# Kernel optimization log

Measured on AMD Instinct MI355X. Metric: run time of the kernel, lower is better.

Reference implementation:

```python
import jax, jax.numpy as jnp
import numpy as np

D_MODEL = 1024
NUM_HEADS = 16
HEAD_DIM = D_MODEL // NUM_HEADS
MAX_SEQ_LEN = 2048
THETA = 10000.0
B, T = 2, 2048


def precompute_cos_sin(head_dim, max_len, theta):
    freqs = 1.0 / theta ** (jnp.arange(0, head_dim, 2, dtype=jnp.float32) / head_dim)
    t = jnp.arange(max_len, dtype=jnp.float32)
    f = jnp.outer(t, freqs)  # [max_len, head_dim//2]
    return jnp.concatenate([jnp.cos(f), jnp.sin(f)], axis=-1)  # [max_len, head_dim]


def apply_rotary_emb(x, cos_sin):
    # x: [B, H, T, Hs]; cos_sin: [T, Hs]
    xr = x.reshape(*x.shape[:-1], -1, 2)
    x1, x2 = xr[..., 0], xr[..., 1]
    cos, sin = jnp.split(cos_sin, 2, axis=-1)  # each [T, Hs//2]
    out = jnp.stack([x1 * cos - x2 * sin, x1 * sin + x2 * cos], axis=-1)
    return out.reshape(x.shape).astype(x.dtype)


def setup_inputs() -> dict:
    key = jax.random.key(0)
    ks = jax.random.split(key, 5)
    scale = 1.0 / np.sqrt(D_MODEL)
    return {
        'x': jax.random.normal(ks[0], (B, T, D_MODEL), dtype=jnp.float32),
        'wq': jax.random.normal(ks[1], (D_MODEL, D_MODEL), dtype=jnp.float32) * scale,
        'wk': jax.random.normal(ks[2], (D_MODEL, D_MODEL), dtype=jnp.float32) * scale,
        'wv': jax.random.normal(ks[3], (D_MODEL, D_MODEL), dtype=jnp.float32) * scale,
        'wo': jax.random.normal(ks[4], (D_MODEL, D_MODEL), dtype=jnp.float32) * scale,
    }


def reference(x, wq, wk, wv, wo):
    seq_len = x.shape[1]
    # Linear: einsum('...i,oi->...o'), weight stored as [out, in]
    q = jnp.einsum('bti,oi->bto', x, wq)
    k = jnp.einsum('bti,oi->bto', x, wk)
    v = jnp.einsum('bti,oi->bto', x, wv)
    # split heads: B T (nH Hs) -> B nH T Hs
    def split_heads(t):
        return t.reshape(t.shape[0], t.shape[1], NUM_HEADS, HEAD_DIM).transpose(0, 2, 1, 3)
    xq, xk, xv = split_heads(q), split_heads(k), split_heads(v)
    cos_sin = precompute_cos_sin(HEAD_DIM, MAX_SEQ_LEN, THETA)[:seq_len]
    xq = apply_rotary_emb(xq, cos_sin)
    xk = apply_rotary_emb(xk, cos_sin)
    scores = jnp.einsum('bhqd,bhkd->bhqk', xq, xk) / jnp.sqrt(jnp.float32(HEAD_DIM))
    causal = jnp.tril(jnp.ones((seq_len, seq_len), dtype=bool))
    scores = jnp.where(causal[None, None], scores, -jnp.inf)
    attn = jax.nn.softmax(scores, axis=-1)
    xo = jnp.einsum('bhqk,bhkd->bhqd', attn, xv)
    xo = xo.transpose(0, 2, 1, 3).reshape(x.shape[0], seq_len, D_MODEL)
    return jnp.einsum('bti,oi->bto', xo, wo)
```

## Files before the change

### kernel.cpp

```cpp
#include <hip/hip_runtime.h>
#include <hip/hip_bf16.h>

typedef __hip_bfloat16 bf16;
using s8v = __attribute__((ext_vector_type(8))) short;
using s4v = __attribute__((ext_vector_type(4))) short;
using f4v = __attribute__((ext_vector_type(4))) float;

#define D_MODEL 1024
#define NHEADS  16
#define HDIM    64
#define TSEQ    2048
#define NBATCH  2
#define BT      (NBATCH * TSEQ)

#define QSCALE  0.180336880111f
#define SBIAS  -17.3123404907f

__device__ inline short f2bf_bits(float f) {
    bf16 h = __float2bfloat16(f);
    return *reinterpret_cast<short*>(&h);
}

__device__ inline void load8(const bf16* p, s8v& o) { o = *(const s8v*)p; }
__device__ inline void load8(const float* p, s8v& o) {
    const f4v a = *(const f4v*)p;
    const f4v b = *(const f4v*)(p + 4);
    s8v r;
    r[0] = f2bf_bits(a[0]); r[1] = f2bf_bits(a[1]);
    r[2] = f2bf_bits(a[2]); r[3] = f2bf_bits(a[3]);
    r[4] = f2bf_bits(b[0]); r[5] = f2bf_bits(b[1]);
    r[6] = f2bf_bits(b[2]); r[7] = f2bf_bits(b[3]);
    o = r;
}

__device__ inline void storeC(bf16* p, float v)  { *p = __float2bfloat16(v); }
__device__ inline void storeC(float* p, float v) { *p = v; }

__device__ inline void gload_lds16(const bf16* g, short* l) {
    __builtin_amdgcn_global_load_lds(
        (__attribute__((address_space(1))) void*)(unsigned long long)(size_t)g,
        (__attribute__((address_space(3))) void*)l,
        16, 0, 0);
}

__device__ inline void stage8(const bf16* g, short* l) { gload_lds16(g, l); }
__device__ inline void stage8(const float* g, short* l) {
    s8v v; load8(g, v); *(s8v*)l = v;
}

__global__ __launch_bounds__(256) void cvt_kernel(
    const float* __restrict__ src, bf16* __restrict__ dst)
{
    const size_t i = ((size_t)blockIdx.x * 256 + threadIdx.x) * 8;
    s8v v; load8(src + i, v);
    *(s8v*)&dst[i] = v;
}

__global__ __launch_bounds__(256) void cvt_all_kernel(
    const float* __restrict__ x,  bf16* __restrict__ xb,
    const float* __restrict__ wq, bf16* __restrict__ wqb,
    const float* __restrict__ wk, bf16* __restrict__ wkb,
    const float* __restrict__ wv, bf16* __restrict__ wvb,
    const float* __restrict__ wo, bf16* __restrict__ wob,
    float2* __restrict__ cs_table)
{
    const int blk = blockIdx.x;
    if (blk >= 4096) {
        const int idx = (blk - 4096) * 256 + threadIdx.x;
        const int tt = idx >> 5;
        const int i  = idx & 31;
        const float inv_freq = expf(-(float)i * (9.210340371976184f / 32.0f));
        float s, c;
        sincosf((float)tt * inv_freq, &s, &c);
        cs_table[idx] = make_float2(c, s);
        return;
    }
    const float* src; bf16* dst; int base;
    if (blk < 2048)      { src = x;  dst = xb;  base = 0; }
    else if (blk < 2560) { src = wq; dst = wqb; base = 2048; }
    else if (blk < 3072) { src = wk; dst = wkb; base = 2560; }
    else if (blk < 3584) { src = wv; dst = wvb; base = 3072; }
    else                 { src = wo; dst = wob; base = 3584; }
    const size_t i = ((size_t)(blk - base) * 256 + threadIdx.x) * 8;
    s8v v; load8(src + i, v);
    *(s8v*)&dst[i] = v;
}

template <int TM, bool ROPE, typename TA, typename TW, typename TC>
__global__ __launch_bounds__(256, 2) void gemm_bt(
    const TA* __restrict__ A,
    const TW* __restrict__ W0, const TW* __restrict__ W1, const TW* __restrict__ W2,
    TC* __restrict__ C0, TC* __restrict__ C1, TC* __restrict__ C2,
    bf16* __restrict__ VT, const float2* __restrict__ cs_table)
{
    const TW* W = (blockIdx.z == 0) ? W0 : (blockIdx.z == 1) ? W1 : W2;
    TC*       C = (blockIdx.z == 0) ? C0 : (blockIdx.z == 1) ? C1 : C2;
    const bool vt_mode = (VT != nullptr) && (blockIdx.z == 2);

    constexpr int K = 1024, N = 1024;
    constexpr int MT = TM / 32;
    __shared__ __align__(16) short As[TM * 64];
    __shared__ __align__(16) short Ws[128 * 64];

    const int t    = threadIdx.x;
    const int lane = t & 63;
    const int wave = t >> 6;
    const int m16  = lane & 15;
    const int quad = lane >> 4;
    const int wm   = (wave >> 1) * (TM / 2);
    const int wn   = (wave & 1) * 64;
    const int rowBase = blockIdx.x * TM;
    const int colBase = blockIdx.y * 128;

    f4v acc[MT][4];
#pragma unroll
    for (int i = 0; i < MT; ++i)
#pragma unroll
        for (int j = 0; j < 4; ++j) acc[i][j] = f4v{0.f, 0.f, 0.f, 0.f};

    for (int kk = 0; kk < K / 64; ++kk) {
#pragma unroll
        for (int r = 0; r < TM / 32; ++r) {
            const int chunk = r * 256 + t;
            const int row   = chunk >> 3;
            const int c8s   = (chunk & 7) ^ (row & 7);
            stage8(A + (size_t)(rowBase + row) * K + kk * 64 + c8s * 8, &As[chunk * 8]);
        }
#pragma unroll
        for (int r = 0; r < 4; ++r) {
            const int chunk = r * 256 + t;
            const int row   = chunk >> 3;
            const int c8s   = (chunk & 7) ^ (row & 7);
            stage8(W + (size_t)(colBase + row) * K + kk * 64 + c8s * 8, &Ws[chunk * 8]);
        }
        __syncthreads();

#pragma unroll
        for (int ks = 0; ks < 2; ++ks) {
            s8v af[MT], bw[4];
#pragma unroll
            for (int mt = 0; mt < MT; ++mt) {
                const int rowa = wm + mt * 16 + m16;
                af[mt] = *(const s8v*)&As[rowa * 64 + ((ks * 4 + quad) ^ (rowa & 7)) * 8];
            }
#pragma unroll
            for (int nt = 0; nt < 4; ++nt) {
                const int roww = wn + nt * 16 + m16;
                bw[nt] = *(const s8v*)&Ws[roww * 64 + ((ks * 4 + quad) ^ (roww & 7)) * 8];
            }
#pragma unroll
            for (int mt = 0; mt < MT; ++mt)
#pragma unroll
                for (int nt = 0; nt < 4; ++nt)
                    acc[mt][nt] = __builtin_amdgcn_mfma_f32_16x16x32_bf16(
                        af[mt], bw[nt], acc[mt][nt], 0, 0, 0);
        }
        __syncthreads();
    }

    if (vt_mode) {
#pragma unroll
        for (int mt = 0; mt < MT; ++mt)
#pragma unroll
            for (int nt = 0; nt < 4; ++nt) {
                const int col  = colBase + wn + nt * 16 + m16;
                const int row0 = rowBase + wm + mt * 16 + quad * 4;
                const int bb   = row0 >> 11;
                const int tt   = row0 & (TSEQ - 1);
                s4v pk;
#pragma unroll
                for (int r = 0; r < 4; ++r) pk[r] = f2bf_bits(acc[mt][nt][r]);
                *(s4v*)&VT[((size_t)(bb * 1024 + col)) * TSEQ + tt] = pk;
            }
    } else {
        const float qs = (ROPE && blockIdx.z == 0) ? QSCALE : 1.0f;
#pragma unroll
        for (int mt = 0; mt < MT; ++mt)
#pragma unroll
            for (int nt = 0; nt < 4; ++nt) {
                const int col = colBase + wn + nt * 16 + m16;
#pragma unroll
                for (int r = 0; r < 4; ++r) {
                    const int row = rowBase + wm + mt * 16 + quad * 4 + r;
                    float v = acc[mt][nt][r];
                    if (ROPE) {
                        const float prt = __shfl_xor(v, 1, 64);
                        const int   tt  = row & (TSEQ - 1);
                        const int   i   = (col & 63) >> 1;
                        const float2 cs = cs_table[tt * 32 + i];
                        v = (col & 1) ? (prt * cs.y + v * cs.x)
                                      : (v * cs.x - prt * cs.y);
                        v *= qs;
                    }
                    storeC(&C[(size_t)row * N + col], v);
                }
            }
    }
}

__global__ __launch_bounds__(256) void rope_inplace(
    bf16* __restrict__ qp, bf16* __restrict__ kp)
{
    const int idx = blockIdx.x * 256 + threadIdx.x;
    const int i  = idx & 31;
    const int h  = (idx >> 5) & (NHEADS - 1);
    const int tt = (idx >> 9) & (TSEQ - 1);
    const int b  = idx >> 20;

    const size_t src = (size_t)(b * TSEQ + tt) * D_MODEL + h * HDIM + 2 * i;

    const float inv_freq = expf(-(float)i * (9.210340371976184f / 32.0f));
    const float f = (float)tt * inv_freq;
    float s, c;
    sincosf(f, &s, &c);

    const float q1 = __bfloat162float(qp[src]);
    const float q2 = __bfloat162float(qp[src + 1]);
    qp[src]     = __float2bfloat16((q1 * c - q2 * s) * QSCALE);
    qp[src + 1] = __float2bfloat16((q1 * s + q2 * c) * QSCALE);

    const float k1 = __bfloat162float(kp[src]);
    const float k2 = __bfloat162float(kp[src + 1]);
    kp[src]     = __float2bfloat16(k1 * c - k2 * s);
    kp[src + 1] = __float2bfloat16(k1 * s + k2 * c);
}

__global__ __launch_bounds__(256, 2) void attn_kernel(
    bf16* __restrict__ qp, const bf16* __restrict__ kp,
    const bf16* __restrict__ vt)
{
    const int hb = blockIdx.x & 31;
    const int ib = blockIdx.x >> 5;
    const int h  = hb & (NHEADS - 1);
    const int b  = hb >> 4;
    const int t    = threadIdx.x;
    const int lane = t & 63;
    const int wave = t >> 6;
    const int m16  = lane & 15;
    const int quad = lane >> 4;

    bf16*       Qb  = qp + (size_t)b * TSEQ * D_MODEL + h * HDIM;
    const bf16* Kb  = kp + (size_t)b * TSEQ * D_MODEL + h * HDIM;
    const bf16* Vtb = vt + ((size_t)b * 1024 + h * HDIM) * TSEQ;

    __shared__ __align__(16) short Klds[2][128 * 64];
    __shared__ __align__(16) short Vlds[2][64 * 128];
    __shared__ __align__(16) short P_lds[4][16 * 128];

    s8v ones;
#pragma unroll
    for (int j = 0; j < 8; ++j) ones[j] = (short)0x3F80;

    auto stage_kv = [&](int buf, int kv0) {
#pragma unroll
        for (int r = 0; r < 4; ++r) {
            const int chunk = r * 256 + t;
            const int row   = chunk >> 3;
            const int c8s   = (chunk & 7) ^ (row & 7);
            gload_lds16(Kb + (size_t)(kv0 + row) * D_MODEL + c8s * 8,
                        &Klds[buf][chunk * 8]);
        }
#pragma unroll
        for (int r = 0; r < 4; ++r) {
            const int chunk = r * 256 + t;
            const int row   = chunk >> 4;
            const int c16s  = (chunk & 15) ^ (row & 15);
            gload_lds16(Vtb + (size_t)row * TSEQ + kv0 + c16s * 8,
                        &Vlds[buf][chunk * 8]);
        }
    };

#pragma unroll 1
    for (int pass = 0; pass < 2; ++pass) {
        const int bx = pass ? (31 - ib) : ib;
        const int q0 = bx * 64 + wave * 16;

        const s8v aq0 = *(const s8v*)&Qb[(size_t)(q0 + m16) * D_MODEL + quad * 8];
        const s8v aq1 = *(const s8v*)&Qb[(size_t)(q0 + m16) * D_MODEL + 32 + quad * 8];

        f4v o_acc[4];
#pragma unroll
        for (int nd = 0; nd < 4; ++nd) o_acc[nd] = f4v{0.f, 0.f, 0.f, 0.f};
        f4v o_l = f4v{0.f, 0.f, 0.f, 0.f};

        const int iters = (bx + 2) >> 1;

        stage_kv(0, 0);

#pragma unroll 1
        for (int it = 0; it < iters; ++it) {
            const int cur = it & 1;
            const int kv0 = it * 128;

            if (it + 1 < iters) {
                stage_kv(cur ^ 1, kv0 + 128);
                asm volatile("s_waitcnt vmcnt(8)" ::: "memory");
            } else {
                asm volatile("s_waitcnt vmcnt(0)" ::: "memory");
            }
            __builtin_amdgcn_s_barrier();
            __builtin_amdgcn_sched_barrier(0);

            f4v s_acc[8];
#pragma unroll
            for (int nk = 0; nk < 8; ++nk)
                s_acc[nk] = f4v{SBIAS, SBIAS, SBIAS, SBIAS};
            __builtin_amdgcn_s_setprio(1);
#pragma unroll
            for (int nk = 0; nk < 8; ++nk) {
                const int rowk = nk * 16 + m16;
                const int sw   = m16 & 7;
                const s8v bk0 = *(const s8v*)&Klds[cur][rowk * 64 + (quad ^ sw) * 8];
                const s8v bk1 = *(const s8v*)&Klds[cur][rowk * 64 + ((4 + quad) ^ sw) * 8];
                s_acc[nk] = __builtin_amdgcn_mfma_f32_16x16x32_bf16(aq0, bk0, s_acc[nk], 0, 0, 0);
                s_acc[nk] = __builtin_amdgcn_mfma_f32_16x16x32_bf16(aq1, bk1, s_acc[nk], 0, 0, 0);
            }
            __builtin_amdgcn_s_setprio(0);

            const bool diag = (it == iters - 1);
#pragma unroll
            for (int nk = 0; nk < 8; ++nk) {
                const int kv = kv0 + nk * 16 + m16;
#pragma unroll
                for (int r = 0; r < 4; ++r) {
                    float p = __builtin_amdgcn_exp2f(s_acc[nk][r]);
                    if (diag) {
                        const int qi = q0 + quad * 4 + r;
                        p = (kv <= qi) ? p : 0.0f;
                    }
                    const int prow = quad * 4 + r;
                    const int pchk = (nk * 2 + (m16 >> 3)) ^ (prow & 7);
                    P_lds[wave][prow * 128 + (pchk << 3) + (m16 & 7)] = f2bf_bits(p);
                }
            }
            asm volatile("s_waitcnt lgkmcnt(0)" ::: "memory");

            __builtin_amdgcn_s_setprio(1);
#pragma unroll
            for (int kt = 0; kt < 4; ++kt) {
                const int achk = (kt * 4 + quad) ^ (m16 & 7);
                const s8v ap = *(const s8v*)&P_lds[wave][m16 * 128 + (achk << 3)];
#pragma unroll
                for (int nd = 0; nd < 4; ++nd) {
                    const int rowv = nd * 16 + m16;
                    const s8v bv = *(const s8v*)&Vlds[cur][rowv * 128
                                                      + ((kt * 4 + quad) ^ m16) * 8];
                    o_acc[nd] = __builtin_amdgcn_mfma_f32_16x16x32_bf16(
                        ap, bv, o_acc[nd], 0, 0, 0);
                }
                o_l = __builtin_amdgcn_mfma_f32_16x16x32_bf16(ap, ones, o_l, 0, 0, 0);
            }
            __builtin_amdgcn_s_setprio(0);

            asm volatile("s_waitcnt lgkmcnt(0)" ::: "memory");
            __builtin_amdgcn_s_barrier();
        }

        float inv_l[4];
#pragma unroll
        for (int r = 0; r < 4; ++r) inv_l[r] = 1.0f / o_l[r];
#pragma unroll
        for (int nd = 0; nd < 4; ++nd)
#pragma unroll
            for (int r = 0; r < 4; ++r) {
                const int qi = q0 + quad * 4 + r;
                Qb[(size_t)qi * D_MODEL + nd * 16 + m16] =
                    __float2bfloat16(o_acc[nd][r] * inv_l[r]);
            }
    }
}

extern "C" void kernel_launch(void* const* d_in, const int* in_sizes, int n_in,
                              void* d_out, int out_size, void* d_ws, size_t ws_size,
                              hipStream_t stream) {
    const float* x  = (const float*)d_in[0];
    const float* wq = (const float*)d_in[1];
    const float* wk = (const float*)d_in[2];
    const float* wv = (const float*)d_in[3];
    const float* wo = (const float*)d_in[4];
    float* out = (float*)d_out;

    bf16* ws = (bf16*)d_ws;
    const size_t SZ  = (size_t)BT * D_MODEL;
    const size_t SZW = (size_t)D_MODEL * D_MODEL;
    bf16* qp  = ws + 0 * SZ;
    bf16* kp  = ws + 1 * SZ;
    bf16* vt  = (bf16*)d_out;
    bf16* xb  = (bf16*)(out + 2 * 1024 * 1024);

    const size_t need_w    = (2 * SZ + 4 * SZW) * sizeof(bf16);
    const size_t need_full = need_w + 65536 * sizeof(float2);

    if (ws_size >= need_full) {
        bf16*   wqb = ws + 2 * SZ + 0 * SZW;
        bf16*   wkb = ws + 2 * SZ + 1 * SZW;
        bf16*   wvb = ws + 2 * SZ + 2 * SZW;
        bf16*   wob = ws + 2 * SZ + 3 * SZW;
        float2* cst = (float2*)(ws + 2 * SZ + 4 * SZW);

        cvt_all_kernel<<<dim3(4352), 256, 0, stream>>>(
            x, xb, wq, wqb, wk, wkb, wv, wvb, wo, wob, cst);
        gemm_bt<128, true, bf16, bf16, bf16><<<dim3(32, 8, 3), 256, 0, stream>>>(
            xb, wqb, wkb, wvb, qp, kp, qp , vt, cst);
        attn_kernel<<<dim3(512), 256, 0, stream>>>(qp, kp, vt);
        gemm_bt<64, false, bf16, bf16, float><<<dim3(64, 8, 1), 256, 0, stream>>>(
            qp, wob, wob, wob, out, out, out, nullptr, nullptr);
    } else if (ws_size >= need_w) {
        bf16* wqb = ws + 2 * SZ + 0 * SZW;
        bf16* wkb = ws + 2 * SZ + 1 * SZW;
        bf16* wvb = ws + 2 * SZ + 2 * SZW;
        bf16* wob = ws + 2 * SZ + 3 * SZW;
        cvt_all_kernel<<<dim3(4096), 256, 0, stream>>>(
            x, xb, wq, wqb, wk, wkb, wv, wvb, wo, wob, nullptr);
        gemm_bt<128, false, bf16, bf16, bf16><<<dim3(32, 8, 3), 256, 0, stream>>>(
            xb, wqb, wkb, wvb, qp, kp, qp , vt, nullptr);
        rope_inplace<<<dim3(8192), 256, 0, stream>>>(qp, kp);
        attn_kernel<<<dim3(512), 256, 0, stream>>>(qp, kp, vt);
        gemm_bt<64, false, bf16, bf16, float><<<dim3(64, 8, 1), 256, 0, stream>>>(
            qp, wob, wob, wob, out, out, out, nullptr, nullptr);
    } else {
        bf16* wob = kp;
        cvt_kernel<<<dim3(2048), 256, 0, stream>>>(x, xb);
        gemm_bt<128, false, bf16, float, bf16><<<dim3(32, 8, 3), 256, 0, stream>>>(
            xb, wq, wk, wv, qp, kp, qp , vt, nullptr);
        rope_inplace<<<dim3(8192), 256, 0, stream>>>(qp, kp);
        attn_kernel<<<dim3(512), 256, 0, stream>>>(qp, kp, vt);
        cvt_kernel<<<dim3(512), 256, 0, stream>>>(wo, wob);
        gemm_bt<64, false, bf16, bf16, float><<<dim3(64, 8, 1), 256, 0, stream>>>(
            qp, wob, wob, wob, out, out, out, nullptr, nullptr);
    }
}
```

Before: 166.4 us.

## Rework attention kernel to 32x32 MFMA with register-resident P and split-KV waves

The attention kernel now uses 32x32x16 bf16 MFMAs. The four waves are arranged as 2 query groups by 2 KV halves, and S is computed transposed (K as the A operand) so the exponentiated P stays in registers. P is packed to bf16 with v_cvt_pk_bf16_f32 and rearranged with v_permlane32_swap instead of a round trip through P_lds, which also removes the LDS wait between the two GEMMs. The row sum is accumulated in scalar registers rather than with an extra MFMA against a ones vector. The two KV-half partial outputs and sums are combined through shared memory at the end of each pass, adding extra barriers and an LDS reduction.

New measurement: 169.8 us. 2.0% more time.

```diff
diff --git a/kernel.cpp b/kernel.cpp
--- a/kernel.cpp
+++ b/kernel.cpp
@@ -5,6 +5,7 @@
 using s8v = __attribute__((ext_vector_type(8))) short;
 using s4v = __attribute__((ext_vector_type(4))) short;
 using f4v = __attribute__((ext_vector_type(4))) float;
+using f16v = __attribute__((ext_vector_type(16))) float;
 
 #define D_MODEL 1024
 #define NHEADS  16
@@ -19,6 +20,16 @@
 __device__ inline short f2bf_bits(float f) {
     bf16 h = __float2bfloat16(f);
     return *reinterpret_cast<short*>(&h);
+}
+
+__device__ inline unsigned cvt_pk_bf16(float lo, float hi) {
+    unsigned r;
+    asm("v_cvt_pk_bf16_f32 %0, %1, %2" : "=v"(r) : "v"(lo), "v"(hi));
+    return r;
+}
+
+__device__ inline void perm_swap(unsigned &a, unsigned &b) {
+    asm volatile("v_permlane32_swap_b32 %0, %1" : "+v"(a), "+v"(b));
 }
 
 __device__ inline void load8(const bf16* p, s8v& o) { o = *(const s8v*)p; }
@@ -236,8 +247,10 @@
     const int t    = threadIdx.x;
     const int lane = t & 63;
     const int wave = t >> 6;
-    const int m16  = lane & 15;
-    const int quad = lane >> 4;
+    const int l31  = lane & 31;
+    const int hi   = lane >> 5;
+    const int wq   = wave >> 1;
+    const int wk   = wave & 1;
 
     bf16*       Qb  = qp + (size_t)b * TSEQ * D_MODEL + h * HDIM;
     const bf16* Kb  = kp + (size_t)b * TSEQ * D_MODEL + h * HDIM;
@@ -245,11 +258,6 @@
 
     __shared__ __align__(16) short Klds[2][128 * 64];
     __shared__ __align__(16) short Vlds[2][64 * 128];
-    __shared__ __align__(16) short P_lds[4][16 * 128];
-
-    s8v ones;
-#pragma unroll
-    for (int j = 0; j < 8; ++j) ones[j] = (short)0x3F80;
 
     auto stage_kv = [&](int buf, int kv0) {
 #pragma unroll
@@ -273,15 +281,21 @@
 #pragma unroll 1
     for (int pass = 0; pass < 2; ++pass) {
         const int bx = pass ? (31 - ib) : ib;
-        const int q0 = bx * 64 + wave * 16;
-
-        const s8v aq0 = *(const s8v*)&Qb[(size_t)(q0 + m16) * D_MODEL + quad * 8];
-        const s8v aq1 = *(const s8v*)&Qb[(size_t)(q0 + m16) * D_MODEL + 32 + quad * 8];
-
-        f4v o_acc[4];
-#pragma unroll
-        for (int nd = 0; nd < 4; ++nd) o_acc[nd] = f4v{0.f, 0.f, 0.f, 0.f};
-        f4v o_l = f4v{0.f, 0.f, 0.f, 0.f};
+        const int q0 = bx * 64;
+        const int qrow = q0 + wq * 32 + l31;
+
+        const bf16* qptr = Qb + (size_t)qrow * D_MODEL;
+        s8v qf[4];
+#pragma unroll
+        for (int s2 = 0; s2 < 4; ++s2)
+            qf[s2] = *(const s8v*)&qptr[s2 * 16 + hi * 8];
+
+        f16v o_acc[2];
+#pragma unroll
+        for (int db = 0; db < 2; ++db)
+#pragma unroll
+            for (int r = 0; r < 16; ++r) o_acc[db][r] = 0.0f;
+        float l_acc = 0.0f;
 
         const int iters = (bx + 2) >> 1;
 
@@ -301,54 +315,64 @@
             __builtin_amdgcn_s_barrier();
             __builtin_amdgcn_sched_barrier(0);
 
-            f4v s_acc[8];
-#pragma unroll
-            for (int nk = 0; nk < 8; ++nk)
-                s_acc[nk] = f4v{SBIAS, SBIAS, SBIAS, SBIAS};
+            f16v sacc[2];
             __builtin_amdgcn_s_setprio(1);
 #pragma unroll
-            for (int nk = 0; nk < 8; ++nk) {
-                const int rowk = nk * 16 + m16;
-                const int sw   = m16 & 7;
-                const s8v bk0 = *(const s8v*)&Klds[cur][rowk * 64 + (quad ^ sw) * 8];
-                const s8v bk1 = *(const s8v*)&Klds[cur][rowk * 64 + ((4 + quad) ^ sw) * 8];
-                s_acc[nk] = __builtin_amdgcn_mfma_f32_16x16x32_bf16(aq0, bk0, s_acc[nk], 0, 0, 0);
-                s_acc[nk] = __builtin_amdgcn_mfma_f32_16x16x32_bf16(aq1, bk1, s_acc[nk], 0, 0, 0);
+            for (int kb = 0; kb < 2; ++kb) {
+                const int rowk = wk * 64 + kb * 32 + l31;
+                const short* kbase = &Klds[cur][rowk * 64];
+                const int r7 = rowk & 7;
+                f16v acc;
+#pragma unroll
+                for (int r = 0; r < 16; ++r) acc[r] = SBIAS;
+#pragma unroll
+                for (int s2 = 0; s2 < 4; ++s2) {
+                    const s8v ak = *(const s8v*)&kbase[((s2 * 2 + hi) ^ r7) * 8];
+                    acc = __builtin_amdgcn_mfma_f32_32x32x16_bf16(
+                        ak, qf[s2], acc, 0, 0, 0);
+                }
+                sacc[kb] = acc;
             }
             __builtin_amdgcn_s_setprio(0);
 
             const bool diag = (it == iters - 1);
 #pragma unroll
-            for (int nk = 0; nk < 8; ++nk) {
-                const int kv = kv0 + nk * 16 + m16;
-#pragma unroll
-                for (int r = 0; r < 4; ++r) {
-                    float p = __builtin_amdgcn_exp2f(s_acc[nk][r]);
+            for (int kb = 0; kb < 2; ++kb) {
+#pragma unroll
+                for (int r = 0; r < 16; ++r) {
+                    float p = __builtin_amdgcn_exp2f(sacc[kb][r]);
                     if (diag) {
-                        const int qi = q0 + quad * 4 + r;
-                        p = (kv <= qi) ? p : 0.0f;
+                        const int kg = kv0 + wk * 64 + kb * 32
+                                     + (r & 3) + 8 * (r >> 2) + 4 * hi;
+                        p = (kg <= qrow) ? p : 0.0f;
                     }
-                    const int prow = quad * 4 + r;
-                    const int pchk = (nk * 2 + (m16 >> 3)) ^ (prow & 7);
-                    P_lds[wave][prow * 128 + (pchk << 3) + (m16 & 7)] = f2bf_bits(p);
+                    sacc[kb][r] = p;
+                    l_acc += p;
                 }
             }
-            asm volatile("s_waitcnt lgkmcnt(0)" ::: "memory");
 
             __builtin_amdgcn_s_setprio(1);
 #pragma unroll
-            for (int kt = 0; kt < 4; ++kt) {
-                const int achk = (kt * 4 + quad) ^ (m16 & 7);
-                const s8v ap = *(const s8v*)&P_lds[wave][m16 * 128 + (achk << 3)];
-#pragma unroll
-                for (int nd = 0; nd < 4; ++nd) {
-                    const int rowv = nd * 16 + m16;
-                    const s8v bv = *(const s8v*)&Vlds[cur][rowv * 128
-                                                      + ((kt * 4 + quad) ^ m16) * 8];
-                    o_acc[nd] = __builtin_amdgcn_mfma_f32_16x16x32_bf16(
-                        ap, bv, o_acc[nd], 0, 0, 0);
+            for (int s = 0; s < 4; ++s) {
+                const int kb = s >> 1;
+                const int h8 = (s & 1) * 8;
+                unsigned w0 = cvt_pk_bf16(sacc[kb][h8 + 0], sacc[kb][h8 + 1]);
+                unsigned w1 = cvt_pk_bf16(sacc[kb][h8 + 2], sacc[kb][h8 + 3]);
+                unsigned w2 = cvt_pk_bf16(sacc[kb][h8 + 4], sacc[kb][h8 + 5]);
+                unsigned w3 = cvt_pk_bf16(sacc[kb][h8 + 6], sacc[kb][h8 + 7]);
+                perm_swap(w0, w2);
+                perm_swap(w1, w3);
+                union { unsigned u[4]; s8v v; } pu;
+                pu.u[0] = w0; pu.u[1] = w1; pu.u[2] = w2; pu.u[3] = w3;
+                const int gch = wk * 8 + s * 2 + hi;
+#pragma unroll
+                for (int db = 0; db < 2; ++db) {
+                    const int rowd = db * 32 + l31;
+                    const s8v bv = *(const s8v*)&Vlds[cur][rowd * 128
+                                                    + (gch ^ (rowd & 15)) * 8];
+                    o_acc[db] = __builtin_amdgcn_mfma_f32_32x32x16_bf16(
+                        pu.v, bv, o_acc[db], 0, 0, 0);
                 }
-                o_l = __builtin_amdgcn_mfma_f32_16x16x32_bf16(ap, ones, o_l, 0, 0, 0);
             }
             __builtin_amdgcn_s_setprio(0);
 
@@ -356,17 +380,40 @@
             __builtin_amdgcn_s_barrier();
         }
 
-        float inv_l[4];
-#pragma unroll
-        for (int r = 0; r < 4; ++r) inv_l[r] = 1.0f / o_l[r];
-#pragma unroll
-        for (int nd = 0; nd < 4; ++nd)
-#pragma unroll
-            for (int r = 0; r < 4; ++r) {
-                const int qi = q0 + quad * 4 + r;
-                Qb[(size_t)qi * D_MODEL + nd * 16 + m16] =
-                    __float2bfloat16(o_acc[nd][r] * inv_l[r]);
-            }
+        const float lw = l_acc + __shfl_xor(l_acc, 32, 64);
+        float* Xf = (float*)&Klds[0][0];
+        float* Lf = (float*)&Vlds[0][0];
+        __syncthreads();
+
+        {
+            const f16v* opw = (wk == 0) ? &o_acc[1] : &o_acc[0];
+#pragma unroll
+            for (int r = 0; r < 16; ++r) {
+                const int qo = (r & 3) + 8 * (r >> 2) + 4 * hi;
+                Xf[((wq * 2 + wk) * 32 + qo) * 32 + l31] = (*opw)[r];
+            }
+        }
+        if (lane < 32) Lf[(wq * 2 + wk) * 32 + l31] = lw;
+        __syncthreads();
+
+        {
+            const f16v* opm = (wk == 0) ? &o_acc[0] : &o_acc[1];
+#pragma unroll
+            for (int rg = 0; rg < 4; ++rg) {
+                const f4v lp0 = *(const f4v*)&Lf[(wq * 2 + 0) * 32 + rg * 8 + hi * 4];
+                const f4v lp1 = *(const f4v*)&Lf[(wq * 2 + 1) * 32 + rg * 8 + hi * 4];
+#pragma unroll
+                for (int j = 0; j < 4; ++j) {
+                    const int r  = rg * 4 + j;
+                    const int qo = rg * 8 + hi * 4 + j;
+                    const float oo = (*opm)[r]
+                        + Xf[((wq * 2 + (1 - wk)) * 32 + qo) * 32 + l31];
+                    Qb[(size_t)(q0 + wq * 32 + qo) * D_MODEL + wk * 32 + l31] =
+                        __float2bfloat16(oo / (lp0[j] + lp1[j]));
+                }
+            }
+        }
+        __syncthreads();
     }
 }
 
```
